# Optimization experiments

Hardware: AMD Instinct MI355X
Metric: run time of the kernel (lower is better)

The kernel has to match this reference:

```python
import jax, jax.numpy as jnp
import numpy as np

N = 50000       # nodes
E = 800000      # edges (before self-loops)
F_IN = 128      # per-head input features (nfeat * t_size, t_size=1)
NHID = 128
NHEADS = 4
NCLASS = 64
NEG_SLOPE = 0.2   # GATConv leakyrelu negative_slope
ALPHA = 0.2       # outer LeakyReLU(alpha)


def setup_inputs():
    key = jax.random.key(0)
    ks = jax.random.split(key, 10)
    type_emb = jax.random.normal(ks[0], (NHEADS, N, F_IN), jnp.float32)
    edge = jax.random.randint(ks[1], (2, E), 0, N, dtype=jnp.int32)
    W = jax.random.normal(ks[2], (NHEADS, F_IN, NHID), jnp.float32) / np.sqrt(F_IN).astype(np.float32)
    att_src = jax.random.normal(ks[3], (NHEADS, NHID), jnp.float32) * 0.1
    att_dst = jax.random.normal(ks[4], (NHEADS, NHID), jnp.float32) * 0.1
    bias = jnp.zeros((NHEADS, NHID), jnp.float32)
    W_out = jax.random.normal(ks[5], (NHID * NHEADS, NCLASS), jnp.float32) / np.sqrt(NHID * NHEADS).astype(np.float32)
    att_src_out = jax.random.normal(ks[6], (NCLASS,), jnp.float32) * 0.1
    att_dst_out = jax.random.normal(ks[7], (NCLASS,), jnp.float32) * 0.1
    bias_out = jnp.zeros((NCLASS,), jnp.float32)
    return {"type_emb": type_emb, "edge": edge, "W": W, "att_src": att_src,
            "att_dst": att_dst, "bias": bias, "W_out": W_out,
            "att_src_out": att_src_out, "att_dst_out": att_dst_out,
            "bias_out": bias_out}


def _gat_conv(x, src, dst, W, a_src, a_dst, b):
    """PyG GATConv, heads=1, with self-loops already in (src, dst)."""
    xs = x @ W                                      # [N, H]
    e = jax.nn.leaky_relu((xs @ a_src)[src] + (xs @ a_dst)[dst], NEG_SLOPE)  # [E']
    # segment softmax over destination nodes (every node has a self-loop -> no empty segment)
    m = jax.ops.segment_max(e, dst, num_segments=N)
    ex = jnp.exp(e - m[dst])
    denom = jax.ops.segment_sum(ex, dst, num_segments=N)
    alpha = ex / denom[dst]                          # [E']
    out = jax.ops.segment_sum(alpha[:, None] * xs[src], dst, num_segments=N)  # [N, H]
    return out + b


def reference(type_emb, edge, W, att_src, att_dst, bias, W_out,
              att_src_out, att_dst_out, bias_out):
    loop = jnp.arange(N, dtype=edge.dtype)
    src = jnp.concatenate([edge[0], loop])
    dst = jnp.concatenate([edge[1], loop])
    # per-head GraphAttentionLayer: GATConv -> LeakyReLU(alpha) (dropout inactive)
    heads = [jax.nn.leaky_relu(
                 _gat_conv(type_emb[i], src, dst, W[i], att_src[i], att_dst[i], bias[i]),
                 ALPHA)
             for i in range(NHEADS)]
    x = jnp.concatenate(heads, axis=1)               # [N, NHID*NHEADS]
    y = jax.nn.leaky_relu(
            _gat_conv(x, src, dst, W_out, att_src_out, att_dst_out, bias_out),
            ALPHA)
    return jnp.tanh(y)                               # [N, NCLASS]
```

## Files before the change

### kernel.cpp

```cpp
#include <hip/hip_runtime.h>
#include <cmath>

#define NN 50000
#define EE 800000
#define ETOT (EE + NN)
#define NSCAN ((NN + 1023) / 1024)
#define SROWS 50048

typedef __bf16 v8bf __attribute__((ext_vector_type(8)));
typedef float f32x4 __attribute__((ext_vector_type(4)));
typedef float f32x2 __attribute__((ext_vector_type(2)));

__device__ __forceinline__ float lrelu(float x){ return x > 0.0f ? x : 0.2f * x; }
__device__ __forceinline__ unsigned short f2bf_rne(float x){
  unsigned int u = __float_as_uint(x);
  u += 0x7fffu + ((u >> 16) & 1u);
  return (unsigned short)(u >> 16);
}
__device__ __forceinline__ float bf2f(unsigned short b){
  return __uint_as_float(((unsigned int)b) << 16);
}
__device__ __forceinline__ void fma8p(f32x2* acc, float w, uint4 u){
  f32x2 w2 = {w, w};
  f32x2 a0, a1, a2, a3;
  a0[0] = __uint_as_float(u.x << 16); a0[1] = __uint_as_float(u.x & 0xffff0000u);
  a1[0] = __uint_as_float(u.y << 16); a1[1] = __uint_as_float(u.y & 0xffff0000u);
  a2[0] = __uint_as_float(u.z << 16); a2[1] = __uint_as_float(u.z & 0xffff0000u);
  a3[0] = __uint_as_float(u.w << 16); a3[1] = __uint_as_float(u.w & 0xffff0000u);
  acc[0] += w2 * a0;
  acc[1] += w2 * a1;
  acc[2] += w2 * a2;
  acc[3] += w2 * a3;
}

__global__ void k_hist(const int* __restrict__ dst, int* __restrict__ cnt){
  int i = blockIdx.x * 256 + threadIdx.x;
  if (i >= ETOT) return;
  int d = (i < EE) ? dst[i] : (i - EE);
  atomicAdd(&cnt[d], 1);
}

__global__ void k_scan1(const int* __restrict__ cnt, int* __restrict__ part){
  __shared__ int sm[256];
  int b = blockIdx.x, t = threadIdx.x;
  int base = b * 1024 + t * 4;
  int s = 0;
  #pragma unroll
  for (int j = 0; j < 4; j++) if (base + j < NN) s += cnt[base + j];
  sm[t] = s; __syncthreads();
  for (int off = 128; off; off >>= 1){
    if (t < off) sm[t] += sm[t + off];
    __syncthreads();
  }
  if (t == 0) part[b] = sm[0];
}

__global__ void k_scan2(const int* __restrict__ part, int* __restrict__ part2){
  if (threadIdx.x == 0 && blockIdx.x == 0){
    int run = 0;
    for (int i = 0; i < NSCAN; i++){ part2[i] = run; run += part[i]; }
  }
}

__global__ void k_scan3(const int* __restrict__ cnt, const int* __restrict__ part2,
                        int* __restrict__ rowptr){
  __shared__ int sm[256];
  int b = blockIdx.x, t = threadIdx.x;
  int base = b * 1024 + t * 4;
  int v[4]; int s = 0;
  #pragma unroll
  for (int j = 0; j < 4; j++){ v[j] = (base + j < NN) ? cnt[base + j] : 0; s += v[j]; }
  sm[t] = s; __syncthreads();
  for (int off = 1; off < 256; off <<= 1){
    int x = (t >= off) ? sm[t - off] : 0;
    __syncthreads();
    sm[t] += x;
    __syncthreads();
  }
  int run = part2[b] + sm[t] - s;
  #pragma unroll
  for (int j = 0; j < 4; j++){
    if (base + j < NN){ rowptr[base + j] = run; run += v[j]; }
  }
  if (b == 0 && t == 0) rowptr[NN] = ETOT;
}

__global__ void k_scatter(const int* __restrict__ src, const int* __restrict__ dst,
                          const int* __restrict__ rowptr, int* __restrict__ fill,
                          int* __restrict__ csr){
  int i = blockIdx.x * 256 + threadIdx.x;
  if (i >= ETOT) return;
  int s, d;
  if (i < EE){ s = src[i]; d = dst[i]; } else { s = d = i - EE; }
  int pos = rowptr[d] + atomicAdd(&fill[d], 1);
  csr[pos] = s;
}

__global__ void k_convB(const float* __restrict__ B, unsigned short* __restrict__ bh,
                        unsigned short* __restrict__ bl, int K, int N, int total){
  int i = blockIdx.x * 256 + threadIdx.x;
  if (i >= total) return;
  int per = K * N;
  int h = i / per, rem = i - h * per;
  int k = rem / N, n = rem - k * N;
  float x = B[i];
  unsigned short hb = f2bf_rne(x);
  unsigned short lb = f2bf_rne(x - bf2f(hb));
  size_t o = (size_t)h * per + ((size_t)(k >> 3) * N + n) * 8 + (k & 7);
  bh[o] = hb; bl[o] = lb;
}

template<int BN, int OSTR>
__global__ __launch_bounds__(256) void gemm_split(const float* __restrict__ A,
                                                  const unsigned short* __restrict__ Bh,
                                                  const unsigned short* __restrict__ Bl,
                                                  unsigned short* __restrict__ out,
                                                  int M, int K,
                                                  const float* __restrict__ att_s,
                                                  const float* __restrict__ att_d,
                                                  float* __restrict__ ssrc,
                                                  float* __restrict__ sdst){
  const int t = threadIdx.x;
  const int wv = t >> 6, lane = t & 63;
  const int m0 = blockIdx.x * 128;
  const int h = blockIdx.y;
  A  += (size_t)h * M * K;
  Bh += (size_t)h * (K >> 3) * BN * 8;
  Bl += (size_t)h * (K >> 3) * BN * 8;
  const int colOff = h * BN;

  __shared__ v8bf sAh[4][128];
  __shared__ v8bf sAl[4][128];
  __shared__ v8bf sBh[4][BN];
  __shared__ v8bf sBl[4][BN];

  f32x4 acc[2][BN / 16];
  #pragma unroll
  for (int i = 0; i < 2; i++)
    #pragma unroll
    for (int j = 0; j < BN / 16; j++){
      f32x4 z = {0.f, 0.f, 0.f, 0.f};
      acc[i][j] = z;
    }

  const int mRow = t & 127;
  const int kh = (t >> 7) * 16;
  const bool valid = (m0 + mRow) < M;
  const int q = lane >> 4, lm = lane & 15;

  for (int k0 = 0; k0 < K; k0 += 32){
    const float* ap = A + (size_t)(m0 + mRow) * K + k0 + kh;
    float4 v0, v1, v2, v3;
    if (valid){
      v0 = *(const float4*)(ap);
      v1 = *(const float4*)(ap + 4);
      v2 = *(const float4*)(ap + 8);
      v3 = *(const float4*)(ap + 12);
    } else {
      v0 = v1 = v2 = v3 = make_float4(0.f, 0.f, 0.f, 0.f);
    }
    #pragma unroll
    for (int g = 0; g < 2; g++){
      float xv[8];
      if (g == 0){ xv[0]=v0.x; xv[1]=v0.y; xv[2]=v0.z; xv[3]=v0.w; xv[4]=v1.x; xv[5]=v1.y; xv[6]=v1.z; xv[7]=v1.w; }
      else       { xv[0]=v2.x; xv[1]=v2.y; xv[2]=v2.z; xv[3]=v2.w; xv[4]=v3.x; xv[5]=v3.y; xv[6]=v3.z; xv[7]=v3.w; }
      v8bf H, L;
      #pragma unroll
      for (int i = 0; i < 8; i++){
        __bf16 hb = (__bf16)xv[i];
        float  hf = (float)hb;
        H[i] = hb;
        L[i] = (__bf16)(xv[i] - hf);
      }
      int k8 = (kh >> 3) + g;
      sAh[k8][mRow] = H;
      sAl[k8][mRow] = L;
    }
    {
      const v8bf* gh = (const v8bf*)Bh + (size_t)(k0 >> 3) * BN;
      const v8bf* gl = (const v8bf*)Bl + (size_t)(k0 >> 3) * BN;
      v8bf* dh = &sBh[0][0];
      v8bf* dl = &sBl[0][0];
      #pragma unroll
      for (int i = t; i < 4 * BN; i += 256){ dh[i] = gh[i]; dl[i] = gl[i]; }
    }
    __syncthreads();
    v8bf ah[2], al[2];
    #pragma unroll
    for (int rt = 0; rt < 2; rt++){
      int m = wv * 32 + rt * 16 + lm;
      ah[rt] = sAh[q][m];
      al[rt] = sAl[q][m];
    }
    #pragma unroll
    for (int ct = 0; ct < BN / 16; ct++){
      v8bf bh = sBh[q][ct * 16 + lm];
      v8bf bl = sBl[q][ct * 16 + lm];
      #pragma unroll
      for (int rt = 0; rt < 2; rt++){
        acc[rt][ct] = __builtin_amdgcn_mfma_f32_16x16x32_bf16(ah[rt], bh, acc[rt][ct], 0, 0, 0);
        acc[rt][ct] = __builtin_amdgcn_mfma_f32_16x16x32_bf16(ah[rt], bl, acc[rt][ct], 0, 0, 0);
        acc[rt][ct] = __builtin_amdgcn_mfma_f32_16x16x32_bf16(al[rt], bh, acc[rt][ct], 0, 0, 0);
      }
    }
    __syncthreads();
  }

  float asv[BN / 16], adv[BN / 16];
  #pragma unroll
  for (int ct = 0; ct < BN / 16; ct++){
    asv[ct] = att_s[h * BN + ct * 16 + lm];
    adv[ct] = att_d[h * BN + ct * 16 + lm];
  }

  #pragma unroll
  for (int rt = 0; rt < 2; rt++){
    #pragma unroll
    for (int reg = 0; reg < 4; reg++){
      int r = m0 + wv * 32 + rt * 16 + q * 4 + reg;
      float d0 = 0.f, d1 = 0.f;
      #pragma unroll
      for (int ct = 0; ct < BN / 16; ct++){
        float v = acc[rt][ct][reg];
        d0 += v * asv[ct];
        d1 += v * adv[ct];
      }
      #pragma unroll
      for (int off = 1; off < 16; off <<= 1){
        d0 += __shfl_xor(d0, off, 64);
        d1 += __shfl_xor(d1, off, 64);
      }
      if (r < M){
        unsigned short* orow = out + (size_t)r * OSTR + colOff + lm;
        #pragma unroll
        for (int ct = 0; ct < BN / 16; ct++)
          orow[ct * 16] = f2bf_rne(acc[rt][ct][reg]);
        if (lm == 0){
          ssrc[(size_t)h * SROWS + r] = d0;
          sdst[(size_t)h * SROWS + r] = d1;
        }
      }
    }
  }
}

template<int BN, int OSTR>
__global__ __launch_bounds__(256) void gemm_ps(const unsigned short* __restrict__ Ah,
                                               const unsigned short* __restrict__ Al,
                                               const unsigned short* __restrict__ Bh,
                                               const unsigned short* __restrict__ Bl,
                                               unsigned short* __restrict__ out,
                                               int M, int K,
                                               const float* __restrict__ att_s,
                                               const float* __restrict__ att_d,
                                               float* __restrict__ ssrc,
                                               float* __restrict__ sdst){
  const int t = threadIdx.x;
  const int wv = t >> 6, lane = t & 63;
  const int m0 = blockIdx.x * 128;
  const int h = blockIdx.y;
  const int colOff = h * BN;

  __shared__ v8bf sAh[4][128];
  __shared__ v8bf sAl[4][128];
  __shared__ v8bf sBh[4][BN];
  __shared__ v8bf sBl[4][BN];

  f32x4 acc[2][BN / 16];
  #pragma unroll
  for (int i = 0; i < 2; i++)
    #pragma unroll
    for (int j = 0; j < BN / 16; j++){
      f32x4 z = {0.f, 0.f, 0.f, 0.f};
      acc[i][j] = z;
    }

  const int mRow = t & 127;
  const int kh = (t >> 7) * 16;
  const bool valid = (m0 + mRow) < M;
  const int q = lane >> 4, lm = lane & 15;

  for (int k0 = 0; k0 < K; k0 += 32){
    const unsigned short* aph = Ah + (size_t)(m0 + mRow) * K + k0 + kh;
    const unsigned short* apl = Al + (size_t)(m0 + mRow) * K + k0 + kh;
    uint4 h0, h1, l0, l1;
    if (valid){
      h0 = *(const uint4*)(aph);
      h1 = *(const uint4*)(aph + 8);
      l0 = *(const uint4*)(apl);
      l1 = *(const uint4*)(apl + 8);
    } else {
      h0 = h1 = l0 = l1 = make_uint4(0, 0, 0, 0);
    }
    int k8 = kh >> 3;
    sAh[k8][mRow]     = *(v8bf*)&h0;
    sAh[k8 + 1][mRow] = *(v8bf*)&h1;
    sAl[k8][mRow]     = *(v8bf*)&l0;
    sAl[k8 + 1][mRow] = *(v8bf*)&l1;
    {
      const v8bf* gh = (const v8bf*)Bh + (size_t)(k0 >> 3) * BN;
      const v8bf* gl = (const v8bf*)Bl + (size_t)(k0 >> 3) * BN;
      v8bf* dh = &sBh[0][0];
      v8bf* dl = &sBl[0][0];
      #pragma unroll
      for (int i = t; i < 4 * BN; i += 256){ dh[i] = gh[i]; dl[i] = gl[i]; }
    }
    __syncthreads();
    v8bf ah[2], al[2];
    #pragma unroll
    for (int rt = 0; rt < 2; rt++){
      int m = wv * 32 + rt * 16 + lm;
      ah[rt] = sAh[q][m];
      al[rt] = sAl[q][m];
    }
    #pragma unroll
    for (int ct = 0; ct < BN / 16; ct++){
      v8bf bh = sBh[q][ct * 16 + lm];
      v8bf bl = sBl[q][ct * 16 + lm];
      #pragma unroll
      for (int rt = 0; rt < 2; rt++){
        acc[rt][ct] = __builtin_amdgcn_mfma_f32_16x16x32_bf16(ah[rt], bh, acc[rt][ct], 0, 0, 0);
        acc[rt][ct] = __builtin_amdgcn_mfma_f32_16x16x32_bf16(ah[rt], bl, acc[rt][ct], 0, 0, 0);
        acc[rt][ct] = __builtin_amdgcn_mfma_f32_16x16x32_bf16(al[rt], bh, acc[rt][ct], 0, 0, 0);
      }
    }
    __syncthreads();
  }

  float asv[BN / 16], adv[BN / 16];
  #pragma unroll
  for (int ct = 0; ct < BN / 16; ct++){
    asv[ct] = att_s[h * BN + ct * 16 + lm];
    adv[ct] = att_d[h * BN + ct * 16 + lm];
  }

  #pragma unroll
  for (int rt = 0; rt < 2; rt++){
    #pragma unroll
    for (int reg = 0; reg < 4; reg++){
      int r = m0 + wv * 32 + rt * 16 + q * 4 + reg;
      float d0 = 0.f, d1 = 0.f;
      #pragma unroll
      for (int ct = 0; ct < BN / 16; ct++){
        float v = acc[rt][ct][reg];
        d0 += v * asv[ct];
        d1 += v * adv[ct];
      }
      #pragma unroll
      for (int off = 1; off < 16; off <<= 1){
        d0 += __shfl_xor(d0, off, 64);
        d1 += __shfl_xor(d1, off, 64);
      }
      if (r < M){
        unsigned short* orow = out + (size_t)r * OSTR + colOff + lm;
        #pragma unroll
        for (int ct = 0; ct < BN / 16; ct++)
          orow[ct * 16] = f2bf_rne(acc[rt][ct][reg]);
        if (lm == 0){
          ssrc[(size_t)h * SROWS + r] = d0;
          sdst[(size_t)h * SROWS + r] = d1;
        }
      }
    }
  }
}

__global__ __launch_bounds__(256) void k_agg1(const int* __restrict__ rowptr,
                                              const int* __restrict__ csr,
                                              const float* __restrict__ ssrc,
                                              const float* __restrict__ sdst,
                                              const unsigned short* __restrict__ xs_all,
                                              const float* __restrict__ bias,
                                              unsigned short* __restrict__ x1h,
                                              unsigned short* __restrict__ x1l){
  int tid = blockIdx.x * 256 + threadIdx.x;
  int n = tid >> 4;
  int lm = threadIdx.x & 15;
  int h = blockIdx.y;
  if (n >= NN) return;
  int start = rowptr[n], end = rowptr[n + 1];
  const float* sp = ssrc + (size_t)h * SROWS;
  float sdn = sdst[(size_t)h * SROWS + n];
  const uint4* xp = (const uint4*)xs_all + h * 16 + lm;

  float sloc = 0.f;
  f32x2 acc[4];
  #pragma unroll
  for (int i = 0; i < 4; i++){ f32x2 z = {0.f, 0.f}; acc[i] = z; }

  int e = start;
  int sA = csr[e];
  float svA = sp[sA];
  uint4 uA = xp[(size_t)sA * 64];
  for (; e + 1 < end; e++){
    int sB = csr[e + 1];
    float svB = sp[sB];
    uint4 uB = xp[(size_t)sB * 64];
    float w = __expf(lrelu(svA + sdn));
    sloc += w;
    fma8p(acc, w, uA);
    svA = svB; uA = uB;
  }
  float w = __expf(lrelu(svA + sdn));
  sloc += w;
  fma8p(acc, w, uA);

  float inv = 1.f / sloc;

  const float* bp = bias + h * 128 + lm * 8;
  float4 b0 = *(const float4*)bp, b1 = *(const float4*)(bp + 4);
  float bb[8] = {b0.x, b0.y, b0.z, b0.w, b1.x, b1.y, b1.z, b1.w};
  union { uint4 q; unsigned short u[8]; } HH, LL;
  #pragma unroll
  for (int i = 0; i < 8; i++){
    float o = lrelu(acc[i >> 1][i & 1] * inv + bb[i]);
    unsigned short hb = f2bf_rne(o);
    HH.u[i] = hb;
    LL.u[i] = f2bf_rne(o - bf2f(hb));
  }
  size_t ofs = (size_t)n * 512 + h * 128 + lm * 8;
  *(uint4*)(x1h + ofs) = HH.q;
  *(uint4*)(x1l + ofs) = LL.q;
}

__global__ __launch_bounds__(256) void k_agg2(const int* __restrict__ rowptr,
                                              const int* __restrict__ csr,
                                              const float* __restrict__ ssrc,
                                              const float* __restrict__ sdst,
                                              const unsigned short* __restrict__ xs2,
                                              const float* __restrict__ bias,
                                              float* __restrict__ outp){
  int tid = blockIdx.x * 256 + threadIdx.x;
  int n = tid >> 3;
  int lm = threadIdx.x & 7;
  if (n >= NN) return;
  int start = rowptr[n], end = rowptr[n + 1];
  float sdn = sdst[n];
  const uint4* xp = (const uint4*)xs2 + lm;

  float sloc = 0.f;
  f32x2 acc[4];
  #pragma unroll
  for (int i = 0; i < 4; i++){ f32x2 z = {0.f, 0.f}; acc[i] = z; }

  int e = start;
  int sA = csr[e];
  float svA = ssrc[sA];
  uint4 uA = xp[(size_t)sA * 8];
  for (; e + 1 < end; e++){
    int sB = csr[e + 1];
    float svB = ssrc[sB];
    uint4 uB = xp[(size_t)sB * 8];
    float w = __expf(lrelu(svA + sdn));
    sloc += w;
    fma8p(acc, w, uA);
    svA = svB; uA = uB;
  }
  float w = __expf(lrelu(svA + sdn));
  sloc += w;
  fma8p(acc, w, uA);

  float inv = 1.f / sloc;

  float o[8];
  #pragma unroll
  for (int i = 0; i < 8; i++)
    o[i] = tanhf(lrelu(acc[i >> 1][i & 1] * inv + bias[lm * 8 + i]));
  float* op = outp + (size_t)n * 64 + lm * 8;
  *(float4*)op       = make_float4(o[0], o[1], o[2], o[3]);
  *(float4*)(op + 4) = make_float4(o[4], o[5], o[6], o[7]);
}

extern "C" void kernel_launch(void* const* d_in, const int* in_sizes, int n_in,
                              void* d_out, int out_size, void* d_ws, size_t ws_size,
                              hipStream_t stream){
  const float* type_emb  = (const float*)d_in[0];
  const int*   edge      = (const int*)d_in[1];
  const float* W         = (const float*)d_in[2];
  const float* att_src   = (const float*)d_in[3];
  const float* att_dst   = (const float*)d_in[4];
  const float* bias      = (const float*)d_in[5];
  const float* W_out     = (const float*)d_in[6];
  const float* att_src_o = (const float*)d_in[7];
  const float* att_dst_o = (const float*)d_in[8];
  const float* bias_o    = (const float*)d_in[9];
  float* out = (float*)d_out;
  (void)in_sizes; (void)n_in; (void)out_size; (void)ws_size;

  char* ws = (char*)d_ws;
  size_t off = 0;
  auto alloc = [&](size_t bytes) -> void* {
    void* p = ws + off;
    off = (off + bytes + 255) & ~(size_t)255;
    return p;
  };
  unsigned short* xs_all = (unsigned short*)alloc((size_t)NN * 512 * 2);
  unsigned short* x1h    = (unsigned short*)alloc((size_t)NN * 512 * 2);
  unsigned short* x1l    = (unsigned short*)alloc((size_t)NN * 512 * 2);
  unsigned short* xs2    = (unsigned short*)alloc((size_t)NN * 64 * 2);
  float* ssrc1 = (float*)alloc((size_t)4 * SROWS * 4);
  float* sdst1 = (float*)alloc((size_t)4 * SROWS * 4);
  float* ssrc2 = (float*)alloc((size_t)SROWS * 4);
  float* sdst2 = (float*)alloc((size_t)SROWS * 4);
  int* cnt    = (int*)alloc((size_t)NN * 4);
  int* rowptr = (int*)alloc((size_t)(NN + 1) * 4);
  int* fill   = (int*)alloc((size_t)NN * 4);
  int* csr    = (int*)alloc((size_t)ETOT * 4);
  int* p1     = (int*)alloc((size_t)NSCAN * 4 + 256);
  int* p2     = (int*)alloc((size_t)NSCAN * 4 + 256);
  unsigned short* Bh1 = (unsigned short*)alloc((size_t)4 * 128 * 128 * 2);
  unsigned short* Bl1 = (unsigned short*)alloc((size_t)4 * 128 * 128 * 2);
  unsigned short* Bh2 = (unsigned short*)alloc((size_t)512 * 64 * 2);
  unsigned short* Bl2 = (unsigned short*)alloc((size_t)512 * 64 * 2);

  hipMemsetAsync(cnt, 0, (size_t)NN * 4, stream);
  hipMemsetAsync(fill, 0, (size_t)NN * 4, stream);
  k_hist<<<(ETOT + 255) / 256, 256, 0, stream>>>(edge + EE, cnt);
  k_scan1<<<NSCAN, 256, 0, stream>>>(cnt, p1);
  k_scan2<<<1, 64, 0, stream>>>(p1, p2);
  k_scan3<<<NSCAN, 256, 0, stream>>>(cnt, p2, rowptr);
  k_scatter<<<(ETOT + 255) / 256, 256, 0, stream>>>(edge, edge + EE, rowptr, fill, csr);

  k_convB<<<(4 * 128 * 128 + 255) / 256, 256, 0, stream>>>(W, Bh1, Bl1, 128, 128, 4 * 128 * 128);
  k_convB<<<(512 * 64 + 255) / 256, 256, 0, stream>>>(W_out, Bh2, Bl2, 512, 64, 512 * 64);

  gemm_split<128, 512><<<dim3(391, 4), 256, 0, stream>>>(
      type_emb, Bh1, Bl1, xs_all, NN, 128, att_src, att_dst, ssrc1, sdst1);
  k_agg1<<<dim3(3125, 4), 256, 0, stream>>>(rowptr, csr, ssrc1, sdst1, xs_all, bias, x1h, x1l);

  gemm_ps<64, 64><<<dim3(391, 1), 256, 0, stream>>>(
      x1h, x1l, Bh2, Bl2, xs2, NN, 512, att_src_o, att_dst_o, ssrc2, sdst2);
  k_agg2<<<1563, 256, 0, stream>>>(rowptr, csr, ssrc2, sdst2, xs2, bias_o, out);
}
```

Baseline: 457.5 us.

## Stage GEMM epilogue through LDS for coalesced stores; halve aggregation lanes per node

The GEMM epilogues now write the bf16 output tile into a shared-memory buffer that aliases the operand staging area, then store it to global memory with coalesced 32-bit writes instead of scattered 16-bit stores. Both aggregation kernels now give each lane two 16-byte chunks, so there are half as many lanes per node and half as many blocks. This is meant to cut uncoalesced store traffic and the per-edge overhead of the index and score loads, which each lane repeated. The cost is an extra barrier in the GEMM, more registers per lane, and fewer warps in flight to hide gather latency.

Measured after the change: 492.7 us. 7.7% more time.

```diff
diff --git a/kernel.cpp b/kernel.cpp
--- a/kernel.cpp
+++ b/kernel.cpp
@@ -120,6 +120,16 @@
                                                   const float* __restrict__ att_d,
                                                   float* __restrict__ ssrc,
                                                   float* __restrict__ sdst){
+  constexpr int SB_BYTES = 4 * BN * 16;
+  constexpr int SM_BYTES = 16384 + 2 * SB_BYTES;
+  constexpr int CT_BYTES = 128 * BN * 2;
+  constexpr int LDS_BYTES = SM_BYTES > CT_BYTES ? SM_BYTES : CT_BYTES;
+  __shared__ __align__(16) char smem[LDS_BYTES];
+  v8bf (*sAh)[128] = (v8bf(*)[128])(smem);
+  v8bf (*sAl)[128] = (v8bf(*)[128])(smem + 8192);
+  v8bf (*sBh)[BN]  = (v8bf(*)[BN])(smem + 16384);
+  v8bf (*sBl)[BN]  = (v8bf(*)[BN])(smem + 16384 + SB_BYTES);
+
   const int t = threadIdx.x;
   const int wv = t >> 6, lane = t & 63;
   const int m0 = blockIdx.x * 128;
@@ -128,11 +138,6 @@
   Bh += (size_t)h * (K >> 3) * BN * 8;
   Bl += (size_t)h * (K >> 3) * BN * 8;
   const int colOff = h * BN;
-
-  __shared__ v8bf sAh[4][128];
-  __shared__ v8bf sAl[4][128];
-  __shared__ v8bf sBh[4][BN];
-  __shared__ v8bf sBl[4][BN];
 
   f32x4 acc[2][BN / 16];
   #pragma unroll
@@ -230,16 +235,34 @@
         d0 += __shfl_xor(d0, off, 64);
         d1 += __shfl_xor(d1, off, 64);
       }
-      if (r < M){
-        unsigned short* orow = out + (size_t)r * OSTR + colOff + lm;
-        #pragma unroll
-        for (int ct = 0; ct < BN / 16; ct++)
-          orow[ct * 16] = f2bf_rne(acc[rt][ct][reg]);
-        if (lm == 0){
-          ssrc[(size_t)h * SROWS + r] = d0;
-          sdst[(size_t)h * SROWS + r] = d1;
-        }
-      }
+      if (r < M && lm == 0){
+        ssrc[(size_t)h * SROWS + r] = d0;
+        sdst[(size_t)h * SROWS + r] = d1;
+      }
+    }
+  }
+
+  unsigned short* ctile = (unsigned short*)smem;
+  #pragma unroll
+  for (int rt = 0; rt < 2; rt++)
+    #pragma unroll
+    for (int reg = 0; reg < 4; reg++){
+      int lr = wv * 32 + rt * 16 + q * 4 + reg;
+      #pragma unroll
+      for (int ct = 0; ct < BN / 16; ct++)
+        ctile[lr * BN + ct * 16 + lm] = f2bf_rne(acc[rt][ct][reg]);
+    }
+  __syncthreads();
+  {
+    const unsigned int* ct32 = (const unsigned int*)ctile;
+    constexpr int W = BN / 2;
+    constexpr int TOT = 128 * W;
+    #pragma unroll
+    for (int i = t; i < TOT; i += 256){
+      int row = i / W, c2 = i - row * W;
+      int r = m0 + row;
+      if (r < M)
+        *(unsigned int*)(out + (size_t)r * OSTR + colOff + c2 * 2) = ct32[i];
     }
   }
 }
@@ -255,16 +278,21 @@
                                                const float* __restrict__ att_d,
                                                float* __restrict__ ssrc,
                                                float* __restrict__ sdst){
+  constexpr int SB_BYTES = 4 * BN * 16;
+  constexpr int SM_BYTES = 16384 + 2 * SB_BYTES;
+  constexpr int CT_BYTES = 128 * BN * 2;
+  constexpr int LDS_BYTES = SM_BYTES > CT_BYTES ? SM_BYTES : CT_BYTES;
+  __shared__ __align__(16) char smem[LDS_BYTES];
+  v8bf (*sAh)[128] = (v8bf(*)[128])(smem);
+  v8bf (*sAl)[128] = (v8bf(*)[128])(smem + 8192);
+  v8bf (*sBh)[BN]  = (v8bf(*)[BN])(smem + 16384);
+  v8bf (*sBl)[BN]  = (v8bf(*)[BN])(smem + 16384 + SB_BYTES);
+
   const int t = threadIdx.x;
   const int wv = t >> 6, lane = t & 63;
   const int m0 = blockIdx.x * 128;
   const int h = blockIdx.y;
   const int colOff = h * BN;
-
-  __shared__ v8bf sAh[4][128];
-  __shared__ v8bf sAl[4][128];
-  __shared__ v8bf sBh[4][BN];
-  __shared__ v8bf sBl[4][BN];
 
   f32x4 acc[2][BN / 16];
   #pragma unroll
@@ -351,16 +379,34 @@
         d0 += __shfl_xor(d0, off, 64);
         d1 += __shfl_xor(d1, off, 64);
       }
-      if (r < M){
-        unsigned short* orow = out + (size_t)r * OSTR + colOff + lm;
-        #pragma unroll
-        for (int ct = 0; ct < BN / 16; ct++)
-          orow[ct * 16] = f2bf_rne(acc[rt][ct][reg]);
-        if (lm == 0){
-          ssrc[(size_t)h * SROWS + r] = d0;
-          sdst[(size_t)h * SROWS + r] = d1;
-        }
-      }
+      if (r < M && lm == 0){
+        ssrc[(size_t)h * SROWS + r] = d0;
+        sdst[(size_t)h * SROWS + r] = d1;
+      }
+    }
+  }
+
+  unsigned short* ctile = (unsigned short*)smem;
+  #pragma unroll
+  for (int rt = 0; rt < 2; rt++)
+    #pragma unroll
+    for (int reg = 0; reg < 4; reg++){
+      int lr = wv * 32 + rt * 16 + q * 4 + reg;
+      #pragma unroll
+      for (int ct = 0; ct < BN / 16; ct++)
+        ctile[lr * BN + ct * 16 + lm] = f2bf_rne(acc[rt][ct][reg]);
+    }
+  __syncthreads();
+  {
+    const unsigned int* ct32 = (const unsigned int*)ctile;
+    constexpr int W = BN / 2;
+    constexpr int TOT = 128 * W;
+    #pragma unroll
+    for (int i = t; i < TOT; i += 256){
+      int row = i / W, c2 = i - row * W;
+      int r = m0 + row;
+      if (r < M)
+        *(unsigned int*)(out + (size_t)r * OSTR + colOff + c2 * 2) = ct32[i];
     }
   }
 }
@@ -374,53 +420,55 @@
                                               unsigned short* __restrict__ x1h,
                                               unsigned short* __restrict__ x1l){
   int tid = blockIdx.x * 256 + threadIdx.x;
-  int n = tid >> 4;
-  int lm = threadIdx.x & 15;
+  int n = tid >> 3;
+  int lm = threadIdx.x & 7;
   int h = blockIdx.y;
   if (n >= NN) return;
   int start = rowptr[n], end = rowptr[n + 1];
   const float* sp = ssrc + (size_t)h * SROWS;
   float sdn = sdst[(size_t)h * SROWS + n];
-  const uint4* xp = (const uint4*)xs_all + h * 16 + lm;
+  const uint4* xp = (const uint4*)xs_all + h * 16 + lm * 2;
 
   float sloc = 0.f;
-  f32x2 acc[4];
-  #pragma unroll
-  for (int i = 0; i < 4; i++){ f32x2 z = {0.f, 0.f}; acc[i] = z; }
+  f32x2 acc[8];
+  #pragma unroll
+  for (int i = 0; i < 8; i++){ f32x2 z = {0.f, 0.f}; acc[i] = z; }
 
   int e = start;
   int sA = csr[e];
   float svA = sp[sA];
-  uint4 uA = xp[(size_t)sA * 64];
+  uint4 uA0 = xp[(size_t)sA * 64], uA1 = xp[(size_t)sA * 64 + 1];
   for (; e + 1 < end; e++){
     int sB = csr[e + 1];
     float svB = sp[sB];
-    uint4 uB = xp[(size_t)sB * 64];
+    uint4 uB0 = xp[(size_t)sB * 64], uB1 = xp[(size_t)sB * 64 + 1];
     float w = __expf(lrelu(svA + sdn));
     sloc += w;
-    fma8p(acc, w, uA);
-    svA = svB; uA = uB;
+    fma8p(acc, w, uA0);
+    fma8p(acc + 4, w, uA1);
+    svA = svB; uA0 = uB0; uA1 = uB1;
   }
   float w = __expf(lrelu(svA + sdn));
   sloc += w;
-  fma8p(acc, w, uA);
+  fma8p(acc, w, uA0);
+  fma8p(acc + 4, w, uA1);
 
   float inv = 1.f / sloc;
 
-  const float* bp = bias + h * 128 + lm * 8;
-  float4 b0 = *(const float4*)bp, b1 = *(const float4*)(bp + 4);
-  float bb[8] = {b0.x, b0.y, b0.z, b0.w, b1.x, b1.y, b1.z, b1.w};
-  union { uint4 q; unsigned short u[8]; } HH, LL;
-  #pragma unroll
-  for (int i = 0; i < 8; i++){
-    float o = lrelu(acc[i >> 1][i & 1] * inv + bb[i]);
+  const float* bp = bias + h * 128 + lm * 16;
+  union { uint4 q[2]; unsigned short u[16]; } HH, LL;
+  #pragma unroll
+  for (int i = 0; i < 16; i++){
+    float o = lrelu(acc[i >> 1][i & 1] * inv + bp[i]);
     unsigned short hb = f2bf_rne(o);
     HH.u[i] = hb;
     LL.u[i] = f2bf_rne(o - bf2f(hb));
   }
-  size_t ofs = (size_t)n * 512 + h * 128 + lm * 8;
-  *(uint4*)(x1h + ofs) = HH.q;
-  *(uint4*)(x1l + ofs) = LL.q;
+  size_t ofs = (size_t)n * 512 + h * 128 + lm * 16;
+  *(uint4*)(x1h + ofs)        = HH.q[0];
+  *((uint4*)(x1h + ofs) + 1)  = HH.q[1];
+  *(uint4*)(x1l + ofs)        = LL.q[0];
+  *((uint4*)(x1l + ofs) + 1)  = LL.q[1];
 }
 
 __global__ __launch_bounds__(256) void k_agg2(const int* __restrict__ rowptr,
@@ -431,44 +479,49 @@
                                               const float* __restrict__ bias,
                                               float* __restrict__ outp){
   int tid = blockIdx.x * 256 + threadIdx.x;
-  int n = tid >> 3;
-  int lm = threadIdx.x & 7;
+  int n = tid >> 2;
+  int lm = threadIdx.x & 3;
   if (n >= NN) return;
   int start = rowptr[n], end = rowptr[n + 1];
   float sdn = sdst[n];
-  const uint4* xp = (const uint4*)xs2 + lm;
+  const uint4* xp = (const uint4*)xs2 + lm * 2;
 
   float sloc = 0.f;
-  f32x2 acc[4];
-  #pragma unroll
-  for (int i = 0; i < 4; i++){ f32x2 z = {0.f, 0.f}; acc[i] = z; }
+  f32x2 acc[8];
+  #pragma unroll
+  for (int i = 0; i < 8; i++){ f32x2 z = {0.f, 0.f}; acc[i] = z; }
 
   int e = start;
   int sA = csr[e];
   float svA = ssrc[sA];
-  uint4 uA = xp[(size_t)sA * 8];
+  uint4 uA0 = xp[(size_t)sA * 8], uA1 = xp[(size_t)sA * 8 + 1];
   for (; e + 1 < end; e++){
     int sB = csr[e + 1];
     float svB = ssrc[sB];
-    uint4 uB = xp[(size_t)sB * 8];
+    uint4 uB0 = xp[(size_t)sB * 8], uB1 = xp[(size_t)sB * 8 + 1];
     float w = __expf(lrelu(svA + sdn));
     sloc += w;
-    fma8p(acc, w, uA);
-    svA = svB; uA = uB;
+    fma8p(acc, w, uA0);
+    fma8p(acc + 4, w, uA1);
+    svA = svB; uA0 = uB0; uA1 = uB1;
   }
   float w = __expf(lrelu(svA + sdn));
   sloc += w;
-  fma8p(acc, w, uA);
+  fma8p(acc, w, uA0);
+  fma8p(acc + 4, w, uA1);
 
   float inv = 1.f / sloc;
 
-  float o[8];
-  #pragma unroll
-  for (int i = 0; i < 8; i++)
-    o[i] = tanhf(lrelu(acc[i >> 1][i & 1] * inv + bias[lm * 8 + i]));
-  float* op = outp + (size_t)n * 64 + lm * 8;
-  *(float4*)op       = make_float4(o[0], o[1], o[2], o[3]);
-  *(float4*)(op + 4) = make_float4(o[4], o[5], o[6], o[7]);
+  const float* bp = bias + lm * 16;
+  float o[16];
+  #pragma unroll
+  for (int i = 0; i < 16; i++)
+    o[i] = tanhf(lrelu(acc[i >> 1][i & 1] * inv + bp[i]));
+  float* op = outp + (size_t)n * 64 + lm * 16;
+  *(float4*)op        = make_float4(o[0],  o[1],  o[2],  o[3]);
+  *(float4*)(op + 4)  = make_float4(o[4],  o[5],  o[6],  o[7]);
+  *(float4*)(op + 8)  = make_float4(o[8],  o[9],  o[10], o[11]);
+  *(float4*)(op + 12) = make_float4(o[12], o[13], o[14], o[15]);
 }
 
 extern "C" void kernel_launch(void* const* d_in, const int* in_sizes, int n_in,
@@ -526,9 +579,9 @@
 
   gemm_split<128, 512><<<dim3(391, 4), 256, 0, stream>>>(
       type_emb, Bh1, Bl1, xs_all, NN, 128, att_src, att_dst, ssrc1, sdst1);
-  k_agg1<<<dim3(3125, 4), 256, 0, stream>>>(rowptr, csr, ssrc1, sdst1, xs_all, bias, x1h, x1l);
+  k_agg1<<<dim3(1563, 4), 256, 0, stream>>>(rowptr, csr, ssrc1, sdst1, xs_all, bias, x1h, x1l);
 
   gemm_ps<64, 64><<<dim3(391, 1), 256, 0, stream>>>(
       x1h, x1l, Bh2, Bl2, xs2, NN, 512, att_src_o, att_dst_o, ssrc2, sdst2);
-  k_agg2<<<1563, 256, 0, stream>>>(rowptr, csr, ssrc2, sdst2, xs2, bias_o, out);
-}
+  k_agg2<<<782, 256, 0, stream>>>(rowptr, csr, ssrc2, sdst2, xs2, bias_o, out);
+}
```
